# Kernel tuning notes

Measured on AMD Instinct MI355X. Metric: run time of the kernel, lower is better.

## Reference

```python
import jax, jax.numpy as jnp
import numpy as np

NUM_HEADS = 16
HEAD_DIM = 128
CHUNK = 256
ROPE_BASE = 10000.0


def rotate_half(x):
    x1 = x[..., ::2]
    x2 = x[..., 1::2]
    return jnp.stack((-x2, x1), axis=-1).reshape(x.shape)


def rope_cos_sin(seq_len, head_dim):
    inv_freq = 1.0 / (ROPE_BASE ** (np.arange(0, head_dim, 2, dtype=np.float32) / head_dim))
    pos = np.arange(seq_len, dtype=np.float32)
    freqs = np.outer(pos, inv_freq)                  # [S, D/2]
    emb = np.concatenate([freqs, freqs], axis=-1)    # [S, D]
    return jnp.asarray(np.cos(emb)), jnp.asarray(np.sin(emb))


def setup_inputs() -> dict:
    key = jax.random.key(0)
    k1, k2, k3 = jax.random.split(key, 3)
    B, S, E = 2, 4096, 2048
    x = jax.random.normal(k1, (B, S, E), dtype=jnp.float32)
    W_qkv = jax.random.normal(k2, (3 * E, E), dtype=jnp.float32) * 0.02
    W_out = jax.random.normal(k3, (E, E), dtype=jnp.float32) * 0.02
    return {"x": x, "W_qkv": W_qkv, "W_out": W_out}


def reference(x, W_qkv, W_out):
    B, S, E = x.shape
    H, D = NUM_HEADS, HEAD_DIM
    qkv = x @ W_qkv.T                                  # [B,S,3E]
    qkv = qkv.reshape(B, S, 3, H, D).transpose(2, 0, 3, 1, 4)  # [3,B,H,S,D]
    q, k, v = qkv[0], qkv[1], qkv[2]

    cos, sin = rope_cos_sin(S, D)                      # [S,D]
    cos = cos[None, None]
    sin = sin[None, None]
    q = q * cos + rotate_half(q) * sin
    k = k * cos + rotate_half(k) * sin

    # ELU+1 feature map
    q = jax.nn.elu(q) + 1.0
    k = jax.nn.elu(k) + 1.0

    n_chunks = S // CHUNK
    # [n,B,H,C,D]
    to_chunks = lambda t: t.reshape(B, H, n_chunks, CHUNK, D).transpose(2, 0, 1, 3, 4)
    qs, ks, vs = to_chunks(q), to_chunks(k), to_chunks(v)

    tril = jnp.tril(jnp.ones((CHUNK, CHUNK), dtype=x.dtype))  # inclusive causal mask

    def step(carry, qkv_c):
        S_c, Z_c = carry
        qc, kc, vc = qkv_c
        att = jnp.einsum('bhld,bhmd->bhlm', qc, kc) * tril       # intra-chunk causal scores
        num = jnp.einsum('bhlm,bhme->bhle', att, vc) + jnp.einsum('bhld,bhde->bhle', qc, S_c)
        den = att.sum(-1) + jnp.einsum('bhld,bhd->bhl', qc, Z_c)
        S_new = S_c + jnp.einsum('bhld,bhle->bhde', kc, vc)
        Z_new = Z_c + kc.sum(axis=2)
        return (S_new, Z_new), (num, den)

    S0 = jnp.zeros((B, H, D, D), dtype=x.dtype)
    Z0 = jnp.zeros((B, H, D), dtype=x.dtype)
    _, (num, den) = jax.lax.scan(step, (S0, Z0), (qs, ks, vs))
    # num: [n,B,H,C,D] -> [B,H,S,D]; den: [n,B,H,C] -> [B,H,S]
    num = num.transpose(1, 2, 0, 3, 4).reshape(B, H, S, D)
    den = den.transpose(1, 2, 0, 3).reshape(B, H, S)
    den = jnp.maximum(den, 1e-6)

    out = num / den[..., None]                          # [B,H,S,D]
    out = out.transpose(0, 2, 1, 3).reshape(B, S, H * D)
    return out @ W_out.T
```

## Files before the change

### kernel.cpp

```cpp
#include <hip/hip_runtime.h>
#include <cmath>

#define Ss 4096
#define NCh 16
#define CK 256

typedef unsigned short bfu;
typedef __bf16 bf16x8 __attribute__((ext_vector_type(8)));
typedef float f32x4 __attribute__((ext_vector_type(4)));
typedef unsigned short u16x8 __attribute__((ext_vector_type(8)));

__device__ __forceinline__ float bf2f(unsigned short u) {
    union { unsigned u32; float f; } v; v.u32 = ((unsigned)u) << 16; return v.f;
}
__device__ __forceinline__ unsigned short f2bf(float f) {
    union { float f; unsigned u; } v; v.f = f;
    unsigned r = v.u + 0x7fff + ((v.u >> 16) & 1);
    return (unsigned short)(r >> 16);
}

__device__ __forceinline__ void g2l16(void* lds, const void* g) {
    __builtin_amdgcn_global_load_lds(
        (const __attribute__((address_space(1))) void*)g,
        (__attribute__((address_space(3))) void*)lds, 16, 0, 0);
}

#define MFMA __builtin_amdgcn_mfma_f32_16x16x32_bf16

__global__ void rope_table(float* __restrict__ cosT, float* __restrict__ sinT) {
    int id = blockIdx.x * 256 + threadIdx.x;
    int f = id & 63, s = id >> 6;
    float e = (2.0f * (float)f) / 128.0f;
    float inv = 1.0f / powf(10000.0f, e);
    float ang = (float)s * inv;
    cosT[id] = cosf(ang);
    sinT[id] = sinf(ang);
}

__global__ void conv_bf16(const float* __restrict__ in, bfu* __restrict__ out, int n4) {
    for (int i = blockIdx.x * 256 + threadIdx.x; i < n4; i += gridDim.x * 256) {
        float4 v = ((const float4*)in)[i];
        ushort4 o;
        o.x = f2bf(v.x); o.y = f2bf(v.y); o.z = f2bf(v.z); o.w = f2bf(v.w);
        ((ushort4*)out)[i] = o;
    }
}

template<int EPI>
__global__ __launch_bounds__(512) void gemm256(
    const bfu* __restrict__ A, const bfu* __restrict__ B, int nbx,
    const float* __restrict__ cosT, const float* __restrict__ sinT,
    bfu* __restrict__ qb, bfu* __restrict__ kb,
    bfu* __restrict__ kT, bfu* __restrict__ vT,
    float* __restrict__ outF)
{
    __shared__ bfu AsL[2 * 256 * 64];
    __shared__ bfu BsL[2 * 256 * 64];
    const int nwg = gridDim.x;
    const int q8 = nwg >> 3;
    const int swz = (blockIdx.x & 7) * q8 + (blockIdx.x >> 3);
    const int bm = (swz / nbx) * 256, bn = (swz % nbx) * 256;

    const int tid = threadIdx.x;
    const int wid = tid >> 6, lane = tid & 63;
    const int wm = wid >> 2, wn = wid & 3;
    const int l15 = lane & 15, l7 = lane & 7, lhi = lane >> 4;

    const int rl = tid >> 3;
    const int scol = ((tid & 7) ^ (rl & 7)) * 8;
    const bfu* Ab = A + (size_t)(bm + rl) * 2048 + scol;
    const bfu* Bb = B + (size_t)(bn + rl) * 2048 + scol;

    f32x4 acc[8][4] = {};

    auto stageA = [&](int T) {
        bfu* d = AsL + (T & 1) * 16384 + wid * 512;
        const bfu* s = Ab + (size_t)T * 64;
        g2l16(d,         s);
        g2l16(d + 4096,  s + (size_t)64 * 2048);
        g2l16(d + 8192,  s + (size_t)128 * 2048);
        g2l16(d + 12288, s + (size_t)192 * 2048);
    };
    auto stageB = [&](int T) {
        bfu* d = BsL + (T & 1) * 16384 + wid * 512;
        const bfu* s = Bb + (size_t)T * 64;
        g2l16(d,         s);
        g2l16(d + 4096,  s + (size_t)64 * 2048);
        g2l16(d + 8192,  s + (size_t)128 * 2048);
        g2l16(d + 12288, s + (size_t)192 * 2048);
    };

    stageA(0); stageB(0);
    stageA(1); stageB(1);
    asm volatile("s_waitcnt vmcnt(8)" ::: "memory");
    __builtin_amdgcn_s_barrier();
    asm volatile("" ::: "memory");

    for (int T = 0; T < 32; ++T) {
        const char* Ax = (const char*)AsL + (T & 1) * 32768;
        const char* Bx = (const char*)BsL + (T & 1) * 32768;
        bf16x8 a0[4][2], a1[4][2], b0[2][2], b1[2][2];

#pragma unroll
        for (int mi = 0; mi < 4; ++mi)
#pragma unroll
            for (int ks = 0; ks < 2; ++ks)
                a0[mi][ks] = *(const bf16x8*)(Ax + (wm * 128 + mi * 16 + l15) * 128 + (((ks * 4 + lhi) ^ l7) << 4));
#pragma unroll
        for (int ni = 0; ni < 2; ++ni)
#pragma unroll
            for (int ks = 0; ks < 2; ++ks)
                b0[ni][ks] = *(const bf16x8*)(Bx + (wn * 64 + ni * 16 + l15) * 128 + (((ks * 4 + lhi) ^ l7) << 4));
        asm volatile("s_waitcnt lgkmcnt(0)" ::: "memory");
        __builtin_amdgcn_sched_barrier(0);
        __builtin_amdgcn_s_setprio(1);
#pragma unroll
        for (int mi = 0; mi < 4; ++mi)
#pragma unroll
            for (int ni = 0; ni < 2; ++ni) {
                acc[mi][ni] = MFMA(a0[mi][0], b0[ni][0], acc[mi][ni], 0, 0, 0);
                acc[mi][ni] = MFMA(a0[mi][1], b0[ni][1], acc[mi][ni], 0, 0, 0);
            }
        __builtin_amdgcn_s_setprio(0);

#pragma unroll
        for (int ni = 0; ni < 2; ++ni)
#pragma unroll
            for (int ks = 0; ks < 2; ++ks)
                b1[ni][ks] = *(const bf16x8*)(Bx + (wn * 64 + (ni + 2) * 16 + l15) * 128 + (((ks * 4 + lhi) ^ l7) << 4));
        asm volatile("s_waitcnt lgkmcnt(0)" ::: "memory");
        __builtin_amdgcn_sched_barrier(0);
        __builtin_amdgcn_s_setprio(1);
#pragma unroll
        for (int mi = 0; mi < 4; ++mi)
#pragma unroll
            for (int ni = 0; ni < 2; ++ni) {
                acc[mi][ni + 2] = MFMA(a0[mi][0], b1[ni][0], acc[mi][ni + 2], 0, 0, 0);
                acc[mi][ni + 2] = MFMA(a0[mi][1], b1[ni][1], acc[mi][ni + 2], 0, 0, 0);
            }
        __builtin_amdgcn_s_setprio(0);
        __builtin_amdgcn_s_barrier();
        asm volatile("" ::: "memory");

#pragma unroll
        for (int mi = 0; mi < 4; ++mi)
#pragma unroll
            for (int ks = 0; ks < 2; ++ks)
                a1[mi][ks] = *(const bf16x8*)(Ax + (wm * 128 + (mi + 4) * 16 + l15) * 128 + (((ks * 4 + lhi) ^ l7) << 4));
        if (T < 30) stageB(T + 2);
        asm volatile("s_waitcnt lgkmcnt(0)" ::: "memory");
        __builtin_amdgcn_sched_barrier(0);
        __builtin_amdgcn_s_setprio(1);
#pragma unroll
        for (int mi = 0; mi < 4; ++mi)
#pragma unroll
            for (int ni = 0; ni < 2; ++ni) {
                acc[mi + 4][ni] = MFMA(a1[mi][0], b0[ni][0], acc[mi + 4][ni], 0, 0, 0);
                acc[mi + 4][ni] = MFMA(a1[mi][1], b0[ni][1], acc[mi + 4][ni], 0, 0, 0);
            }
        __builtin_amdgcn_s_setprio(0);
        __builtin_amdgcn_s_barrier();
        asm volatile("" ::: "memory");

        if (T < 30) stageA(T + 2);
        __builtin_amdgcn_s_setprio(1);
#pragma unroll
        for (int mi = 0; mi < 4; ++mi)
#pragma unroll
            for (int ni = 0; ni < 2; ++ni) {
                acc[mi + 4][ni + 2] = MFMA(a1[mi][0], b1[ni][0], acc[mi + 4][ni + 2], 0, 0, 0);
                acc[mi + 4][ni + 2] = MFMA(a1[mi][1], b1[ni][1], acc[mi + 4][ni + 2], 0, 0, 0);
            }
        __builtin_amdgcn_s_setprio(0);
        if (T < 30) { asm volatile("s_waitcnt vmcnt(8)" ::: "memory"); }
        else        { asm volatile("s_waitcnt vmcnt(0)" ::: "memory"); }
        __builtin_amdgcn_s_barrier();
        asm volatile("" ::: "memory");
    }

    if constexpr (EPI == 0) {
        const int part = bn >> 11;
#pragma unroll
        for (int mi = 0; mi < 8; ++mi) {
            const int m0 = bm + wm * 128 + mi * 16 + (lhi << 2);
            const int bq = m0 >> 12;
            const int sloc = m0 & 4095;
#pragma unroll
            for (int ni = 0; ni < 4; ++ni) {
                const int cp = (bn & 2047) + wn * 64 + ni * 16 + l15;
                const int d = cp & 127;
                const int head = cp >> 7;
                const int f = d & 63;
                float vv[4];
#pragma unroll
                for (int r = 0; r < 4; ++r) {
                    float v = acc[mi][ni][r];
                    float p = __shfl_xor(v, 1);
                    if (part < 2) {
                        const int s = (m0 + r) & 4095;
                        float cc = cosT[s * 64 + f], sn = sinT[s * 64 + f];
                        float o = (d & 1) ? v * cc + p * sn : v * cc - p * sn;
                        v = o > 0.0f ? o + 1.0f : __expf(o);
                    }
                    vv[r] = v;
                }
                if (part == 0) {
#pragma unroll
                    for (int r = 0; r < 4; ++r)
                        qb[(size_t)(m0 + r) * 2048 + cp] = f2bf(vv[r]);
                } else if (part == 1) {
#pragma unroll
                    for (int r = 0; r < 4; ++r)
                        kb[(size_t)(m0 + r) * 2048 + cp] = f2bf(vv[r]);
                    ushort4 t4;
                    t4.x = f2bf(vv[0]); t4.y = f2bf(vv[1]); t4.z = f2bf(vv[2]); t4.w = f2bf(vv[3]);
                    *(ushort4*)(kT + ((size_t)(bq * 16 + head) * 128 + d) * 4096 + sloc) = t4;
                } else {
                    ushort4 t4;
                    t4.x = f2bf(vv[0]); t4.y = f2bf(vv[1]); t4.z = f2bf(vv[2]); t4.w = f2bf(vv[3]);
                    *(ushort4*)(vT + ((size_t)(bq * 16 + head) * 128 + d) * 4096 + sloc) = t4;
                }
            }
        }
    } else {
#pragma unroll
        for (int mi = 0; mi < 8; ++mi) {
            const int m0 = bm + wm * 128 + mi * 16 + (lhi << 2);
#pragma unroll
            for (int ni = 0; ni < 4; ++ni) {
                const int n = bn + wn * 64 + ni * 16 + l15;
#pragma unroll
                for (int r = 0; r < 4; ++r)
                    outF[(size_t)(m0 + r) * 2048 + n] = acc[mi][ni][r];
            }
        }
    }
}

__global__ __launch_bounds__(256) void kv_outer_mfma(
    const bfu* __restrict__ vT, const bfu* __restrict__ kT,
    bfu* __restrict__ Scb, float* __restrict__ Zc)
{
    __shared__ bfu As[128 * 64];
    __shared__ bfu Bs[128 * 64];
    __shared__ float zS[128][2];
    const int batch = blockIdx.x;
    const int c = batch & 15, h = (batch >> 4) & 15, b = batch >> 8;
    const size_t fbase = (size_t)(b * 16 + h) * 128 * 4096 + c * 256;
    const int tid = threadIdx.x, wid = tid >> 6, lane = tid & 63;
    const int wr = wid >> 1, wc = wid & 1;
    const int srow = lane >> 3, scol = (lane & 7) * 8;
    f32x4 acc[4][4] = {};
    float zreg = 0.0f;
    const int zd = tid >> 1, zo = (tid & 1) * 32;

    for (int k0 = 0; k0 < 256; k0 += 64) {
        __syncthreads();
#pragma unroll
        for (int i = 0; i < 4; ++i) {
            const int r = i * 32 + wid * 8;
            g2l16(&As[r * 64], vT + fbase + (size_t)(r + srow) * 4096 + k0 + scol);
            g2l16(&Bs[r * 64], kT + fbase + (size_t)(r + srow) * 4096 + k0 + scol);
        }
        __syncthreads();
#pragma unroll
        for (int ks = 0; ks < 2; ++ks) {
            bf16x8 af[4], bfr[4];
#pragma unroll
            for (int mi = 0; mi < 4; ++mi)
                af[mi] = *(const bf16x8*)&As[(wr * 64 + mi * 16 + (lane & 15)) * 64 + ks * 32 + (lane >> 4) * 8];
#pragma unroll
            for (int ni = 0; ni < 4; ++ni)
                bfr[ni] = *(const bf16x8*)&Bs[(wc * 64 + ni * 16 + (lane & 15)) * 64 + ks * 32 + (lane >> 4) * 8];
#pragma unroll
            for (int mi = 0; mi < 4; ++mi)
#pragma unroll
                for (int ni = 0; ni < 4; ++ni)
                    acc[mi][ni] = MFMA(af[mi], bfr[ni], acc[mi][ni], 0, 0, 0);
        }
#pragma unroll
        for (int j = 0; j < 32; ++j) zreg += bf2f(Bs[zd * 64 + zo + j]);
    }
    zS[zd][tid & 1] = zreg;
    __syncthreads();
    if (tid < 128) Zc[(size_t)batch * 128 + tid] = zS[tid][0] + zS[tid][1];
    bfu* Sout = Scb + (size_t)batch * 16384;
#pragma unroll
    for (int mi = 0; mi < 4; ++mi)
#pragma unroll
        for (int ni = 0; ni < 4; ++ni) {
            const int d = wc * 64 + ni * 16 + (lane & 15);
#pragma unroll
            for (int r = 0; r < 4; ++r) {
                const int e = wr * 64 + mi * 16 + ((lane >> 4) << 2) + r;
                Sout[e * 128 + d] = f2bf(acc[mi][ni][r]);
            }
        }
}

__global__ void prefix_Sb(bfu* __restrict__ Scb) {
    size_t idx = (size_t)blockIdx.x * 256 + threadIdx.x;
    size_t bh = idx >> 14, de = idx & 16383;
    bfu* p = Scb + bh * (size_t)NCh * 16384 + de;
    float run = 0.0f;
#pragma unroll
    for (int c = 0; c < NCh; ++c) {
        float t = bf2f(p[(size_t)c * 16384]);
        p[(size_t)c * 16384] = f2bf(run);
        run += t;
    }
}
__global__ void prefix_Z(float* __restrict__ Zc) {
    size_t idx = (size_t)blockIdx.x * 256 + threadIdx.x;
    size_t bh = idx >> 7, d = idx & 127;
    float* p = Zc + bh * (size_t)NCh * 128 + d;
    float run = 0.0f;
#pragma unroll
    for (int c = 0; c < NCh; ++c) {
        float t = p[(size_t)c * 128];
        p[(size_t)c * 128] = run;
        run += t;
    }
}

__global__ __launch_bounds__(256) void chunk_mfma(
    const bfu* __restrict__ qb, const bfu* __restrict__ kb,
    const bfu* __restrict__ vT, const bfu* __restrict__ Scb,
    const float* __restrict__ Zc, bfu* __restrict__ ao)
{
    __shared__ bfu shrd[16384];
    __shared__ bfu attL[16384];
    __shared__ float Zs[128];
    __shared__ float denS[128][2];
    const int half = blockIdx.x, batch = blockIdx.y;
    const int c = batch & 15, h = (batch >> 4) & 15, b = batch >> 8;
    const int row0 = b * Ss + c * CK;
    const int tid = threadIdx.x, wid = tid >> 6, lane = tid & 63;
    const int wr = wid >> 1, wc = wid & 1;
    const int sr = lane >> 4, sc8 = (lane & 15) * 8;
    if (tid < 128) Zs[tid] = Zc[(size_t)batch * 128 + tid];

    bf16x8 qf[4][4];
    {
        const bfu* qrow = qb + (size_t)(row0 + half * 128 + wr * 64 + (lane & 15)) * 2048
                          + h * 128 + (lane >> 4) * 8;
#pragma unroll
        for (int mi = 0; mi < 4; ++mi)
#pragma unroll
            for (int ks = 0; ks < 4; ++ks)
                qf[mi][ks] = *(const bf16x8*)(qrow + (size_t)mi * 16 * 2048 + ks * 32);
    }
    f32x4 num[4][4] = {};
    float den_reg = 0.0f;
    const int dl = tid >> 1, dc0 = (tid & 1) * 64;

    for (int kb_ = 0; kb_ <= half; ++kb_) {
        __syncthreads();
#pragma unroll
        for (int i = 0; i < 8; ++i) {
            const int r = i * 16 + wid * 4;
            g2l16(&shrd[r * 128], kb + (size_t)(row0 + kb_ * 128 + r + sr) * 2048 + h * 128 + sc8);
        }
        __syncthreads();
        f32x4 attacc[4][4] = {};
#pragma unroll
        for (int ks = 0; ks < 4; ++ks) {
            bf16x8 bfr[4];
#pragma unroll
            for (int ni = 0; ni < 4; ++ni)
                bfr[ni] = *(const bf16x8*)&shrd[(wc * 64 + ni * 16 + (lane & 15)) * 128 + ks * 32 + (lane >> 4) * 8];
#pragma unroll
            for (int mi = 0; mi < 4; ++mi)
#pragma unroll
                for (int ni = 0; ni < 4; ++ni)
                    attacc[mi][ni] = MFMA(qf[mi][ks], bfr[ni], attacc[mi][ni], 0, 0, 0);
        }
        __syncthreads();
#pragma unroll
        for (int i = 0; i < 8; ++i) {
            const int r = i * 16 + wid * 4;
            g2l16(&shrd[r * 128],
                  vT + ((size_t)(b * 16 + h) * 128 + r + sr) * 4096 + c * 256 + kb_ * 128 + sc8);
        }
        const bool needmask = (kb_ == half);
#pragma unroll
        for (int mi = 0; mi < 4; ++mi)
#pragma unroll
            for (int ni = 0; ni < 4; ++ni) {
                const int l0 = wr * 64 + mi * 16 + ((lane >> 4) << 2);
                const int m = wc * 64 + ni * 16 + (lane & 15);
#pragma unroll
                for (int r = 0; r < 4; ++r) {
                    const int l = l0 + r;
                    float v = attacc[mi][ni][r];
                    if (needmask && (half * 128 + l) < (kb_ * 128 + m)) v = 0.0f;
                    const int byte = (l * 256 + m * 2) ^ ((l & 7) << 4);
                    *(bfu*)((char*)attL + byte) = f2bf(v);
                }
            }
        __syncthreads();
#pragma unroll
        for (int ks = 0; ks < 4; ++ks) {
            bf16x8 af[4], bfr[4];
#pragma unroll
            for (int mi = 0; mi < 4; ++mi) {
                const int l = wr * 64 + mi * 16 + (lane & 15);
                const int byte = (l * 256 + (ks * 32 + (lane >> 4) * 8) * 2) ^ ((l & 7) << 4);
                af[mi] = *(const bf16x8*)((const char*)attL + byte);
            }
#pragma unroll
            for (int ni = 0; ni < 4; ++ni)
                bfr[ni] = *(const bf16x8*)&shrd[(wc * 64 + ni * 16 + (lane & 15)) * 128 + ks * 32 + (lane >> 4) * 8];
#pragma unroll
            for (int mi = 0; mi < 4; ++mi)
#pragma unroll
                for (int ni = 0; ni < 4; ++ni)
                    num[mi][ni] = MFMA(af[mi], bfr[ni], num[mi][ni], 0, 0, 0);
        }
#pragma unroll
        for (int j8 = 0; j8 < 8; ++j8) {
            const int byte = (dl * 256 + (dc0 + j8 * 8) * 2) ^ ((dl & 7) << 4);
            u16x8 a = *(const u16x8*)((const char*)attL + byte);
#pragma unroll
            for (int jj = 0; jj < 8; ++jj) den_reg += bf2f(a[jj]);
        }
    }
    __syncthreads();
#pragma unroll
    for (int i = 0; i < 8; ++i) {
        const int r = i * 16 + wid * 4;
        g2l16(&shrd[r * 128], Scb + (size_t)batch * 16384 + (size_t)(r + sr) * 128 + sc8);
    }
    __syncthreads();
#pragma unroll
    for (int ks = 0; ks < 4; ++ks) {
        bf16x8 bfr[4];
#pragma unroll
        for (int ni = 0; ni < 4; ++ni)
            bfr[ni] = *(const bf16x8*)&shrd[(wc * 64 + ni * 16 + (lane & 15)) * 128 + ks * 32 + (lane >> 4) * 8];
#pragma unroll
        for (int mi = 0; mi < 4; ++mi)
#pragma unroll
            for (int ni = 0; ni < 4; ++ni)
                num[mi][ni] = MFMA(qf[mi][ks], bfr[ni], num[mi][ni], 0, 0, 0);
    }
    {
        const bfu* qrow = qb + (size_t)(row0 + half * 128 + dl) * 2048 + h * 128 + dc0;
#pragma unroll
        for (int j8 = 0; j8 < 8; ++j8) {
            u16x8 a = *(const u16x8*)(qrow + j8 * 8);
#pragma unroll
            for (int jj = 0; jj < 8; ++jj) den_reg += bf2f(a[jj]) * Zs[dc0 + j8 * 8 + jj];
        }
    }
    denS[dl][tid & 1] = den_reg;
    __syncthreads();
    bfu* aop = ao + (size_t)(row0 + half * 128) * 2048 + h * 128;
#pragma unroll
    for (int mi = 0; mi < 4; ++mi)
#pragma unroll
        for (int ni = 0; ni < 4; ++ni) {
            const int e = wc * 64 + ni * 16 + (lane & 15);
#pragma unroll
            for (int r = 0; r < 4; ++r) {
                const int l = wr * 64 + mi * 16 + ((lane >> 4) << 2) + r;
                float dv = denS[l][0] + denS[l][1];
                dv = dv > 1e-6f ? dv : 1e-6f;
                aop[(size_t)l * 2048 + e] = f2bf(num[mi][ni][r] / dv);
            }
        }
}

extern "C" void kernel_launch(void* const* d_in, const int* in_sizes, int n_in,
                              void* d_out, int out_size, void* d_ws, size_t ws_size,
                              hipStream_t stream)
{
    const float* x    = (const float*)d_in[0];
    const float* Wqkv = (const float*)d_in[1];
    const float* Wout = (const float*)d_in[2];
    float* out = (float*)d_out;
    char* ws = (char*)d_ws;

    bfu* xb   = (bfu*)(ws);
    bfu* ao   = (bfu*)(ws);
    bfu* wqb  = (bfu*)(ws + 33554432);
    bfu* wob  = (bfu*)(ws + 33554432);
    float* cosT = (float*)(ws + 58720256);
    float* sinT = (float*)(ws + 59768832);
    bfu* Scb  = (bfu*)(ws + 60817408);
    float* Zc = (float*)(ws + 77594624);
    bfu* qb   = (bfu*)(ws + 77856768);
    bfu* kb   = (bfu*)(ws + 111411200);
    bfu* kTb  = (bfu*)(ws + 144965632);
    bfu* vTb  = (bfu*)(ws + 178520064);

    rope_table<<<1024, 256, 0, stream>>>(cosT, sinT);
    conv_bf16<<<2048, 256, 0, stream>>>(x,    xb,  4194304);
    conv_bf16<<<2048, 256, 0, stream>>>(Wqkv, wqb, 3145728);
    gemm256<0><<<768, 512, 0, stream>>>(xb, wqb, 24, cosT, sinT, qb, kb, kTb, vTb, nullptr);
    conv_bf16<<<1024, 256, 0, stream>>>(Wout, wob, 1048576);
    kv_outer_mfma<<<512, 256, 0, stream>>>(vTb, kTb, Scb, Zc);
    prefix_Z<<<16, 256, 0, stream>>>(Zc);
    prefix_Sb<<<2048, 256, 0, stream>>>(Scb);
    chunk_mfma<<<dim3(2, 512), 256, 0, stream>>>(qb, kb, vTb, Scb, Zc, ao);
    gemm256<1><<<256, 512, 0, stream>>>(ao, wob, 8, nullptr, nullptr, nullptr, nullptr, nullptr, nullptr, out);
}
```

Before: 471.3 us.

## Software-pipeline LDS fragment reads across MFMA phases in GEMM main loop

Restructures the GEMM main loop so that each LDS fragment read (B1, A1, and the next tile's A0/B0) is issued ahead of the MFMA block that precedes its use. Partial lgkmcnt waits replace full drains, so LDS latency overlaps with matrix math. The stageA prefetch is moved after the final barrier, and a barrier before stageA is removed. Register pressure rises because fragments live across iterations, and the barrier and waitcnt placement becomes more delicate for correctness.

```diff
diff --git a/kernel.cpp b/kernel.cpp
--- a/kernel.cpp
+++ b/kernel.cpp
@@ -72,6 +72,7 @@
     const bfu* Bb = B + (size_t)(bn + rl) * 2048 + scol;
 
     f32x4 acc[8][4] = {};
+    bf16x8 a0[4][2], a1[4][2], b0[2][2], b1[2][2];
 
     auto stageA = [&](int T) {
         bfu* d = AsL + (T & 1) * 16384 + wid * 512;
@@ -89,29 +90,49 @@
         g2l16(d + 8192,  s + (size_t)128 * 2048);
         g2l16(d + 12288, s + (size_t)192 * 2048);
     };
+    auto readA0 = [&](int T) {
+        const char* Ax = (const char*)AsL + (T & 1) * 32768;
+#pragma unroll
+        for (int mi = 0; mi < 4; ++mi)
+#pragma unroll
+            for (int ks = 0; ks < 2; ++ks)
+                a0[mi][ks] = *(const bf16x8*)(Ax + (wm * 128 + mi * 16 + l15) * 128 + (((ks * 4 + lhi) ^ l7) << 4));
+    };
+    auto readB0 = [&](int T) {
+        const char* Bx = (const char*)BsL + (T & 1) * 32768;
+#pragma unroll
+        for (int ni = 0; ni < 2; ++ni)
+#pragma unroll
+            for (int ks = 0; ks < 2; ++ks)
+                b0[ni][ks] = *(const bf16x8*)(Bx + (wn * 64 + ni * 16 + l15) * 128 + (((ks * 4 + lhi) ^ l7) << 4));
+    };
+    auto readB1 = [&](int T) {
+        const char* Bx = (const char*)BsL + (T & 1) * 32768;
+#pragma unroll
+        for (int ni = 0; ni < 2; ++ni)
+#pragma unroll
+            for (int ks = 0; ks < 2; ++ks)
+                b1[ni][ks] = *(const bf16x8*)(Bx + (wn * 64 + (ni + 2) * 16 + l15) * 128 + (((ks * 4 + lhi) ^ l7) << 4));
+    };
+    auto readA1 = [&](int T) {
+        const char* Ax = (const char*)AsL + (T & 1) * 32768;
+#pragma unroll
+        for (int mi = 0; mi < 4; ++mi)
+#pragma unroll
+            for (int ks = 0; ks < 2; ++ks)
+                a1[mi][ks] = *(const bf16x8*)(Ax + (wm * 128 + (mi + 4) * 16 + l15) * 128 + (((ks * 4 + lhi) ^ l7) << 4));
+    };
 
     stageA(0); stageB(0);
     stageA(1); stageB(1);
     asm volatile("s_waitcnt vmcnt(8)" ::: "memory");
     __builtin_amdgcn_s_barrier();
-    asm volatile("" ::: "memory");
+    readA0(0); readB0(0);
+    __builtin_amdgcn_sched_barrier(0);
 
     for (int T = 0; T < 32; ++T) {
-        const char* Ax = (const char*)AsL + (T & 1) * 32768;
-        const char* Bx = (const char*)BsL + (T & 1) * 32768;
-        bf16x8 a0[4][2], a1[4][2], b0[2][2], b1[2][2];
-
-#pragma unroll
-        for (int mi = 0; mi < 4; ++mi)
-#pragma unroll
-            for (int ks = 0; ks < 2; ++ks)
-                a0[mi][ks] = *(const bf16x8*)(Ax + (wm * 128 + mi * 16 + l15) * 128 + (((ks * 4 + lhi) ^ l7) << 4));
-#pragma unroll
-        for (int ni = 0; ni < 2; ++ni)
-#pragma unroll
-            for (int ks = 0; ks < 2; ++ks)
-                b0[ni][ks] = *(const bf16x8*)(Bx + (wn * 64 + ni * 16 + l15) * 128 + (((ks * 4 + lhi) ^ l7) << 4));
-        asm volatile("s_waitcnt lgkmcnt(0)" ::: "memory");
+        readB1(T);
+        asm volatile("s_waitcnt lgkmcnt(12)" ::: "memory");
         __builtin_amdgcn_sched_barrier(0);
         __builtin_amdgcn_s_setprio(1);
 #pragma unroll
@@ -123,12 +144,8 @@
             }
         __builtin_amdgcn_s_setprio(0);
 
-#pragma unroll
-        for (int ni = 0; ni < 2; ++ni)
-#pragma unroll
-            for (int ks = 0; ks < 2; ++ks)
-                b1[ni][ks] = *(const bf16x8*)(Bx + (wn * 64 + (ni + 2) * 16 + l15) * 128 + (((ks * 4 + lhi) ^ l7) << 4));
-        asm volatile("s_waitcnt lgkmcnt(0)" ::: "memory");
+        readA1(T);
+        asm volatile("s_waitcnt lgkmcnt(8)" ::: "memory");
         __builtin_amdgcn_sched_barrier(0);
         __builtin_amdgcn_s_setprio(1);
 #pragma unroll
@@ -139,14 +156,8 @@
                 acc[mi][ni + 2] = MFMA(a0[mi][1], b1[ni][1], acc[mi][ni + 2], 0, 0, 0);
             }
         __builtin_amdgcn_s_setprio(0);
+
         __builtin_amdgcn_s_barrier();
-        asm volatile("" ::: "memory");
-
-#pragma unroll
-        for (int mi = 0; mi < 4; ++mi)
-#pragma unroll
-            for (int ks = 0; ks < 2; ++ks)
-                a1[mi][ks] = *(const bf16x8*)(Ax + (wm * 128 + (mi + 4) * 16 + l15) * 128 + (((ks * 4 + lhi) ^ l7) << 4));
         if (T < 30) stageB(T + 2);
         asm volatile("s_waitcnt lgkmcnt(0)" ::: "memory");
         __builtin_amdgcn_sched_barrier(0);
@@ -158,12 +169,6 @@
                 acc[mi + 4][ni] = MFMA(a1[mi][0], b0[ni][0], acc[mi + 4][ni], 0, 0, 0);
                 acc[mi + 4][ni] = MFMA(a1[mi][1], b0[ni][1], acc[mi + 4][ni], 0, 0, 0);
             }
-        __builtin_amdgcn_s_setprio(0);
-        __builtin_amdgcn_s_barrier();
-        asm volatile("" ::: "memory");
-
-        if (T < 30) stageA(T + 2);
-        __builtin_amdgcn_s_setprio(1);
 #pragma unroll
         for (int mi = 0; mi < 4; ++mi)
 #pragma unroll
@@ -172,10 +177,19 @@
                 acc[mi + 4][ni + 2] = MFMA(a1[mi][1], b1[ni][1], acc[mi + 4][ni + 2], 0, 0, 0);
             }
         __builtin_amdgcn_s_setprio(0);
-        if (T < 30) { asm volatile("s_waitcnt vmcnt(8)" ::: "memory"); }
-        else        { asm volatile("s_waitcnt vmcnt(0)" ::: "memory"); }
+
         __builtin_amdgcn_s_barrier();
-        asm volatile("" ::: "memory");
+        if (T < 30) {
+            stageA(T + 2);
+            asm volatile("s_waitcnt vmcnt(8)" ::: "memory");
+        } else if (T == 30) {
+            asm volatile("s_waitcnt vmcnt(0)" ::: "memory");
+        }
+        if (T < 31) {
+            __builtin_amdgcn_s_barrier();
+            readA0(T + 1); readB0(T + 1);
+            __builtin_amdgcn_sched_barrier(0);
+        }
     }
 
     if constexpr (EPI == 0) {
```

New measurement: 501.4 us. 6.4% more time.

## Interleave GEMM global-to-LDS staging in row granules across MFMA phases

Applied to the files above, without the earlier changes.

The bulk tile loads are split into 64-row granules. Each one is issued in a phase of the K-loop whose LDS region has already been consumed, and the A rows 64/192 for the next tile are prefetched one iteration early. The aim is to spread memory traffic evenly across the four MFMA phases and hide global-load latency better. In exchange it adds extra workgroup barriers per iteration and relies on precise vmcnt accounting, which is fragile.

```diff
diff --git a/kernel.cpp b/kernel.cpp
--- a/kernel.cpp
+++ b/kernel.cpp
@@ -72,45 +72,61 @@
     const bfu* Bb = B + (size_t)(bn + rl) * 2048 + scol;
 
     f32x4 acc[8][4] = {};
-
-    auto stageA = [&](int T) {
-        bfu* d = AsL + (T & 1) * 16384 + wid * 512;
-        const bfu* s = Ab + (size_t)T * 64;
-        g2l16(d,         s);
-        g2l16(d + 4096,  s + (size_t)64 * 2048);
-        g2l16(d + 8192,  s + (size_t)128 * 2048);
-        g2l16(d + 12288, s + (size_t)192 * 2048);
+    bf16x8 a0[4][2], a1[4][2], b0[2][2], b1[2][2];
+
+    auto stA = [&](int T, int r0) {
+        g2l16(AsL + (T & 1) * 16384 + r0 * 64 + wid * 512,
+              Ab + (size_t)r0 * 2048 + (size_t)T * 64);
     };
-    auto stageB = [&](int T) {
-        bfu* d = BsL + (T & 1) * 16384 + wid * 512;
-        const bfu* s = Bb + (size_t)T * 64;
-        g2l16(d,         s);
-        g2l16(d + 4096,  s + (size_t)64 * 2048);
-        g2l16(d + 8192,  s + (size_t)128 * 2048);
-        g2l16(d + 12288, s + (size_t)192 * 2048);
+    auto stB = [&](int T, int r0) {
+        g2l16(BsL + (T & 1) * 16384 + r0 * 64 + wid * 512,
+              Bb + (size_t)r0 * 2048 + (size_t)T * 64);
     };
-
-    stageA(0); stageB(0);
-    stageA(1); stageB(1);
+    auto readA0 = [&](int T) {
+        const char* Ax = (const char*)AsL + (T & 1) * 32768;
+#pragma unroll
+        for (int mi = 0; mi < 4; ++mi)
+#pragma unroll
+            for (int ks = 0; ks < 2; ++ks)
+                a0[mi][ks] = *(const bf16x8*)(Ax + (wm * 128 + mi * 16 + l15) * 128 + (((ks * 4 + lhi) ^ l7) << 4));
+    };
+    auto readB0 = [&](int T) {
+        const char* Bx = (const char*)BsL + (T & 1) * 32768;
+#pragma unroll
+        for (int ni = 0; ni < 2; ++ni)
+#pragma unroll
+            for (int ks = 0; ks < 2; ++ks)
+                b0[ni][ks] = *(const bf16x8*)(Bx + (wn * 64 + ni * 16 + l15) * 128 + (((ks * 4 + lhi) ^ l7) << 4));
+    };
+    auto readB1 = [&](int T) {
+        const char* Bx = (const char*)BsL + (T & 1) * 32768;
+#pragma unroll
+        for (int ni = 0; ni < 2; ++ni)
+#pragma unroll
+            for (int ks = 0; ks < 2; ++ks)
+                b1[ni][ks] = *(const bf16x8*)(Bx + (wn * 64 + (ni + 2) * 16 + l15) * 128 + (((ks * 4 + lhi) ^ l7) << 4));
+    };
+    auto readA1 = [&](int T) {
+        const char* Ax = (const char*)AsL + (T & 1) * 32768;
+#pragma unroll
+        for (int mi = 0; mi < 4; ++mi)
+#pragma unroll
+            for (int ks = 0; ks < 2; ++ks)
+                a1[mi][ks] = *(const bf16x8*)(Ax + (wm * 128 + (mi + 4) * 16 + l15) * 128 + (((ks * 4 + lhi) ^ l7) << 4));
+    };
+
+    stA(0, 0); stA(0, 64); stA(0, 128); stA(0, 192);
+    stB(0, 0); stB(0, 64); stB(0, 128); stB(0, 192);
+    stA(1, 0); stA(1, 64); stA(1, 128); stA(1, 192);
+    stB(1, 0); stB(1, 64); stB(1, 128); stB(1, 192);
     asm volatile("s_waitcnt vmcnt(8)" ::: "memory");
     __builtin_amdgcn_s_barrier();
-    asm volatile("" ::: "memory");
-
-    for (int T = 0; T < 32; ++T) {
-        const char* Ax = (const char*)AsL + (T & 1) * 32768;
-        const char* Bx = (const char*)BsL + (T & 1) * 32768;
-        bf16x8 a0[4][2], a1[4][2], b0[2][2], b1[2][2];
-
-#pragma unroll
-        for (int mi = 0; mi < 4; ++mi)
-#pragma unroll
-            for (int ks = 0; ks < 2; ++ks)
-                a0[mi][ks] = *(const bf16x8*)(Ax + (wm * 128 + mi * 16 + l15) * 128 + (((ks * 4 + lhi) ^ l7) << 4));
-#pragma unroll
-        for (int ni = 0; ni < 2; ++ni)
-#pragma unroll
-            for (int ks = 0; ks < 2; ++ks)
-                b0[ni][ks] = *(const bf16x8*)(Bx + (wn * 64 + ni * 16 + l15) * 128 + (((ks * 4 + lhi) ^ l7) << 4));
+
+    for (int U = 0; U < 32; ++U) {
+        readA0(U); readB0(U);
+        if (U >= 1 && U <= 30) { stA(U + 1, 64); stA(U + 1, 192); }
+        asm volatile("s_waitcnt lgkmcnt(8)" ::: "memory");
+        __builtin_amdgcn_s_barrier();
         asm volatile("s_waitcnt lgkmcnt(0)" ::: "memory");
         __builtin_amdgcn_sched_barrier(0);
         __builtin_amdgcn_s_setprio(1);
@@ -122,12 +138,11 @@
                 acc[mi][ni] = MFMA(a0[mi][1], b0[ni][1], acc[mi][ni], 0, 0, 0);
             }
         __builtin_amdgcn_s_setprio(0);
-
-#pragma unroll
-        for (int ni = 0; ni < 2; ++ni)
-#pragma unroll
-            for (int ks = 0; ks < 2; ++ks)
-                b1[ni][ks] = *(const bf16x8*)(Bx + (wn * 64 + (ni + 2) * 16 + l15) * 128 + (((ks * 4 + lhi) ^ l7) << 4));
+        __builtin_amdgcn_s_barrier();
+
+        readB1(U);
+        if (U < 30) { stA(U + 2, 0); stA(U + 2, 128); }
+        __builtin_amdgcn_s_barrier();
         asm volatile("s_waitcnt lgkmcnt(0)" ::: "memory");
         __builtin_amdgcn_sched_barrier(0);
         __builtin_amdgcn_s_setprio(1);
@@ -140,14 +155,10 @@
             }
         __builtin_amdgcn_s_setprio(0);
         __builtin_amdgcn_s_barrier();
-        asm volatile("" ::: "memory");
-
-#pragma unroll
-        for (int mi = 0; mi < 4; ++mi)
-#pragma unroll
-            for (int ks = 0; ks < 2; ++ks)
-                a1[mi][ks] = *(const bf16x8*)(Ax + (wm * 128 + (mi + 4) * 16 + l15) * 128 + (((ks * 4 + lhi) ^ l7) << 4));
-        if (T < 30) stageB(T + 2);
+
+        readA1(U);
+        if (U < 30) { stB(U + 2, 0); stB(U + 2, 64); }
+        __builtin_amdgcn_s_barrier();
         asm volatile("s_waitcnt lgkmcnt(0)" ::: "memory");
         __builtin_amdgcn_sched_barrier(0);
         __builtin_amdgcn_s_setprio(1);
@@ -160,9 +171,9 @@
             }
         __builtin_amdgcn_s_setprio(0);
         __builtin_amdgcn_s_barrier();
-        asm volatile("" ::: "memory");
-
-        if (T < 30) stageA(T + 2);
+
+        if (U < 30) { stB(U + 2, 128); stB(U + 2, 192); }
+        __builtin_amdgcn_s_barrier();
         __builtin_amdgcn_s_setprio(1);
 #pragma unroll
         for (int mi = 0; mi < 4; ++mi)
@@ -172,10 +183,9 @@
                 acc[mi + 4][ni + 2] = MFMA(a1[mi][1], b1[ni][1], acc[mi + 4][ni + 2], 0, 0, 0);
             }
         __builtin_amdgcn_s_setprio(0);
-        if (T < 30) { asm volatile("s_waitcnt vmcnt(8)" ::: "memory"); }
-        else        { asm volatile("s_waitcnt vmcnt(0)" ::: "memory"); }
-        __builtin_amdgcn_s_barrier();
-        asm volatile("" ::: "memory");
+        if (U < 30)       { asm volatile("s_waitcnt vmcnt(6)" ::: "memory"); }
+        else if (U == 30) { asm volatile("s_waitcnt vmcnt(0)" ::: "memory"); }
+        __builtin_amdgcn_s_barrier();
     }
 
     if constexpr (EPI == 0) {
```

After: 475.1 us. Within noise of the previous version (+0.8%).

## Fuse chunk KV outer products with prefix scan in one per-head kernel

Applied to the files above, without the earlier changes.

The per-chunk K^T V outer-product kernel and the two separate prefix-sum kernels are merged into one kernel with one block per (batch, head). Each block walks the 16 chunks in order and writes the running (exclusive) state before adding the current chunk's contribution in fp32 registers. This removes two launches and the read-modify-write pass over the bf16 state buffer, and it keeps the running sum in fp32 instead of summing bf16 partials. In exchange, parallelism drops from 512 blocks to 32, which leaves most CUs idle during this stage. The two input fp32-to-bf16 conversions are also merged into one launch.

```diff
diff --git a/kernel.cpp b/kernel.cpp
--- a/kernel.cpp
+++ b/kernel.cpp
@@ -37,6 +37,19 @@
     sinT[id] = sinf(ang);
 }
 
+__global__ void conv2_bf16(const float* __restrict__ a, bfu* __restrict__ oa, int n4a,
+                           const float* __restrict__ b, bfu* __restrict__ ob, int n4b) {
+    const int total = n4a + n4b;
+    for (int i = blockIdx.x * 256 + threadIdx.x; i < total; i += gridDim.x * 256) {
+        const float* in; bfu* out; int j;
+        if (i < n4a) { in = a; out = oa; j = i; }
+        else         { in = b; out = ob; j = i - n4a; }
+        float4 v = ((const float4*)in)[j];
+        ushort4 o;
+        o.x = f2bf(v.x); o.y = f2bf(v.y); o.z = f2bf(v.z); o.w = f2bf(v.w);
+        ((ushort4*)out)[j] = o;
+    }
+}
 __global__ void conv_bf16(const float* __restrict__ in, bfu* __restrict__ out, int n4) {
     for (int i = blockIdx.x * 256 + threadIdx.x; i < n4; i += gridDim.x * 256) {
         float4 v = ((const float4*)in)[i];
@@ -237,16 +250,15 @@
     }
 }
 
-__global__ __launch_bounds__(256) void kv_outer_mfma(
+__global__ __launch_bounds__(256) void kv_prefix_mfma(
     const bfu* __restrict__ vT, const bfu* __restrict__ kT,
     bfu* __restrict__ Scb, float* __restrict__ Zc)
 {
     __shared__ bfu As[128 * 64];
     __shared__ bfu Bs[128 * 64];
     __shared__ float zS[128][2];
-    const int batch = blockIdx.x;
-    const int c = batch & 15, h = (batch >> 4) & 15, b = batch >> 8;
-    const size_t fbase = (size_t)(b * 16 + h) * 128 * 4096 + c * 256;
+    const int bh = blockIdx.x;
+    const size_t fb0 = (size_t)bh * 128 * 4096;
     const int tid = threadIdx.x, wid = tid >> 6, lane = tid & 63;
     const int wr = wid >> 1, wc = wid & 1;
     const int srow = lane >> 3, scol = (lane & 7) * 8;
@@ -254,72 +266,54 @@
     float zreg = 0.0f;
     const int zd = tid >> 1, zo = (tid & 1) * 32;
 
-    for (int k0 = 0; k0 < 256; k0 += 64) {
-        __syncthreads();
-#pragma unroll
-        for (int i = 0; i < 4; ++i) {
-            const int r = i * 32 + wid * 8;
-            g2l16(&As[r * 64], vT + fbase + (size_t)(r + srow) * 4096 + k0 + scol);
-            g2l16(&Bs[r * 64], kT + fbase + (size_t)(r + srow) * 4096 + k0 + scol);
-        }
-        __syncthreads();
-#pragma unroll
-        for (int ks = 0; ks < 2; ++ks) {
-            bf16x8 af[4], bfr[4];
-#pragma unroll
-            for (int mi = 0; mi < 4; ++mi)
-                af[mi] = *(const bf16x8*)&As[(wr * 64 + mi * 16 + (lane & 15)) * 64 + ks * 32 + (lane >> 4) * 8];
-#pragma unroll
-            for (int ni = 0; ni < 4; ++ni)
-                bfr[ni] = *(const bf16x8*)&Bs[(wc * 64 + ni * 16 + (lane & 15)) * 64 + ks * 32 + (lane >> 4) * 8];
-#pragma unroll
-            for (int mi = 0; mi < 4; ++mi)
+    for (int c = 0; c < NCh; ++c) {
+        const int batch = bh * NCh + c;
+        bfu* Sout = Scb + (size_t)batch * 16384;
+#pragma unroll
+        for (int mi = 0; mi < 4; ++mi)
+#pragma unroll
+            for (int ni = 0; ni < 4; ++ni) {
+                const int d = wc * 64 + ni * 16 + (lane & 15);
+#pragma unroll
+                for (int r = 0; r < 4; ++r) {
+                    const int e = wr * 64 + mi * 16 + ((lane >> 4) << 2) + r;
+                    Sout[e * 128 + d] = f2bf(acc[mi][ni][r]);
+                }
+            }
+        __syncthreads();
+        zS[zd][tid & 1] = zreg;
+        __syncthreads();
+        if (tid < 128) Zc[(size_t)batch * 128 + tid] = zS[tid][0] + zS[tid][1];
+
+        const size_t fbase = fb0 + (size_t)c * 256;
+        for (int k0 = 0; k0 < 256; k0 += 64) {
+            __syncthreads();
+#pragma unroll
+            for (int i = 0; i < 4; ++i) {
+                const int r = i * 32 + wid * 8;
+                g2l16(&As[r * 64], vT + fbase + (size_t)(r + srow) * 4096 + k0 + scol);
+                g2l16(&Bs[r * 64], kT + fbase + (size_t)(r + srow) * 4096 + k0 + scol);
+            }
+            __syncthreads();
+#pragma unroll
+            for (int ks = 0; ks < 2; ++ks) {
+                bf16x8 af[4], bfr[4];
+#pragma unroll
+                for (int mi = 0; mi < 4; ++mi)
+                    af[mi] = *(const bf16x8*)&As[(wr * 64 + mi * 16 + (lane & 15)) * 64 + ks * 32 + (lane >> 4) * 8];
 #pragma unroll
                 for (int ni = 0; ni < 4; ++ni)
-                    acc[mi][ni] = MFMA(af[mi], bfr[ni], acc[mi][ni], 0, 0, 0);
-        }
-#pragma unroll
-        for (int j = 0; j < 32; ++j) zreg += bf2f(Bs[zd * 64 + zo + j]);
-    }
-    zS[zd][tid & 1] = zreg;
-    __syncthreads();
-    if (tid < 128) Zc[(size_t)batch * 128 + tid] = zS[tid][0] + zS[tid][1];
-    bfu* Sout = Scb + (size_t)batch * 16384;
-#pragma unroll
-    for (int mi = 0; mi < 4; ++mi)
-#pragma unroll
-        for (int ni = 0; ni < 4; ++ni) {
-            const int d = wc * 64 + ni * 16 + (lane & 15);
-#pragma unroll
-            for (int r = 0; r < 4; ++r) {
-                const int e = wr * 64 + mi * 16 + ((lane >> 4) << 2) + r;
-                Sout[e * 128 + d] = f2bf(acc[mi][ni][r]);
-            }
-        }
-}
-
-__global__ void prefix_Sb(bfu* __restrict__ Scb) {
-    size_t idx = (size_t)blockIdx.x * 256 + threadIdx.x;
-    size_t bh = idx >> 14, de = idx & 16383;
-    bfu* p = Scb + bh * (size_t)NCh * 16384 + de;
-    float run = 0.0f;
-#pragma unroll
-    for (int c = 0; c < NCh; ++c) {
-        float t = bf2f(p[(size_t)c * 16384]);
-        p[(size_t)c * 16384] = f2bf(run);
-        run += t;
-    }
-}
-__global__ void prefix_Z(float* __restrict__ Zc) {
-    size_t idx = (size_t)blockIdx.x * 256 + threadIdx.x;
-    size_t bh = idx >> 7, d = idx & 127;
-    float* p = Zc + bh * (size_t)NCh * 128 + d;
-    float run = 0.0f;
-#pragma unroll
-    for (int c = 0; c < NCh; ++c) {
-        float t = p[(size_t)c * 128];
-        p[(size_t)c * 128] = run;
-        run += t;
+                    bfr[ni] = *(const bf16x8*)&Bs[(wc * 64 + ni * 16 + (lane & 15)) * 64 + ks * 32 + (lane >> 4) * 8];
+#pragma unroll
+                for (int mi = 0; mi < 4; ++mi)
+#pragma unroll
+                    for (int ni = 0; ni < 4; ++ni)
+                        acc[mi][ni] = MFMA(af[mi], bfr[ni], acc[mi][ni], 0, 0, 0);
+            }
+#pragma unroll
+            for (int j = 0; j < 32; ++j) zreg += bf2f(Bs[zd * 64 + zo + j]);
+        }
+        __syncthreads();
     }
 }
 
@@ -495,13 +489,10 @@
     bfu* vTb  = (bfu*)(ws + 178520064);
 
     rope_table<<<1024, 256, 0, stream>>>(cosT, sinT);
-    conv_bf16<<<2048, 256, 0, stream>>>(x,    xb,  4194304);
-    conv_bf16<<<2048, 256, 0, stream>>>(Wqkv, wqb, 3145728);
+    conv2_bf16<<<2048, 256, 0, stream>>>(x, xb, 4194304, Wqkv, wqb, 3145728);
     gemm256<0><<<768, 512, 0, stream>>>(xb, wqb, 24, cosT, sinT, qb, kb, kTb, vTb, nullptr);
     conv_bf16<<<1024, 256, 0, stream>>>(Wout, wob, 1048576);
-    kv_outer_mfma<<<512, 256, 0, stream>>>(vTb, kTb, Scb, Zc);
-    prefix_Z<<<16, 256, 0, stream>>>(Zc);
-    prefix_Sb<<<2048, 256, 0, stream>>>(Scb);
+    kv_prefix_mfma<<<32, 256, 0, stream>>>(vTb, kTb, Scb, Zc);
     chunk_mfma<<<dim3(2, 512), 256, 0, stream>>>(qb, kb, vTb, Scb, Zc, ao);
     gemm256<1><<<256, 512, 0, stream>>>(ao, wob, 8, nullptr, nullptr, nullptr, nullptr, nullptr, nullptr, out);
 }
```

Result: slower. 544.6 us (+15.5%).
